# Optimization experiments

Measured on AMD Instinct MI355X. Metric: run time of the kernel, lower is better.

The kernel has to match this reference:

```python
import jax, jax.numpy as jnp
import numpy as np

V_PATCH_NUMS = (1, 2, 4, 6, 8, 10, 13, 16)
HW = 16
QUANT_RESI = 0.5
SHARE_K = 4
BETA = 1.0


def _pool_matrix(n_in, n_out):
    # adaptive average pooling as a [n_out, n_in] matrix (matches F.adaptive_avg_pool2d bins)
    P = np.zeros((n_out, n_in), np.float32)
    for i in range(n_out):
        s = (i * n_in) // n_out
        e = -((-(i + 1) * n_in) // n_out)  # ceil((i+1)*n_in/n_out)
        P[i, s:e] = 1.0 / (e - s)
    return jnp.asarray(P)


def _phi_index(si, SN):
    # PhiPartiallyShared.__getitem__(si/(SN-1)) with K=4 ticks
    K = SHARE_K
    ticks = np.linspace(1.0 / 3 / K, 1 - 1.0 / 3 / K, K) if K == 4 else np.linspace(1.0 / 2 / K, 1 - 1.0 / 2 / K, K)
    return int(np.argmin(np.abs(ticks - si / (SN - 1))))


def _phi(h, w, b):
    # Phi: h*(1-r) + conv3x3(h)*r, zero padding (nn.Conv2d default)
    y = jax.lax.conv_general_dilated(h, w, (1, 1), 'SAME',
                                     dimension_numbers=('NCHW', 'OIHW', 'NCHW'))
    y = y + b[None, :, None, None]
    return h * (1.0 - QUANT_RESI) + y * QUANT_RESI


def setup_inputs() -> dict:
    key = jax.random.key(0)
    k0, k1, k2 = jax.random.split(key, 3)
    B, C, V = 64, 32, 4096
    f = jax.random.normal(k0, (B, C, HW, HW), jnp.float32)
    embed = jax.random.normal(k1, (V, C), jnp.float32)  # EMAEmbedding.weight ~ randn
    phi_w = jax.random.normal(k2, (SHARE_K, C, C, 3, 3), jnp.float32) * (1.0 / np.sqrt(9.0 * C))
    phi_b = jnp.zeros((SHARE_K, C), jnp.float32)
    return {"f_BChw": f, "embed_weight": embed, "phi_w": phi_w, "phi_b": phi_b}


def reference(f_BChw, embed_weight, phi_w, phi_b):
    B, C, H, W = f_BChw.shape
    SN = len(V_PATCH_NUMS)
    f_ng = jax.lax.stop_gradient(f_BChw)
    f_hat = jnp.zeros_like(f_BChw)
    e_sq = jnp.sum(embed_weight * embed_weight, axis=1)  # [V]
    loss = jnp.float32(0.0)
    for si, pn in enumerate(V_PATCH_NUMS):
        rest = f_ng - jax.lax.stop_gradient(f_hat)  # residual to quantize (no grad through distance)
        if pn != H:
            P = _pool_matrix(H, pn)
            rest_d = jnp.einsum('oh,bchw,pw->bcop', P, rest, P)  # adaptive avg pool -> [B,C,pn,pn]
        else:
            rest_d = rest
        rest_NC = rest_d.transpose(0, 2, 3, 1).reshape(-1, C)  # [B*pn*pn, C]
        # squared euclidean cdist to codebook, argmin
        d = (jnp.sum(rest_NC * rest_NC, axis=1, keepdims=True)
             + e_sq[None, :]
             - 2.0 * (rest_NC @ embed_weight.T))  # [N, V]
        idx = jnp.argmin(d, axis=1)  # [B*pn*pn] int
        h = embed_weight[idx].reshape(B, pn, pn, C).transpose(0, 3, 1, 2)  # gather -> [B,C,pn,pn]
        if pn != H:
            h = jax.image.resize(h, (B, C, H, W), method='linear')  # bilinear, align_corners=False
        k = _phi_index(si, SN)
        h = _phi(h, phi_w[k], phi_b[k])
        f_hat = f_hat + h
        loss = loss + 0.25 * jnp.mean((jax.lax.stop_gradient(f_hat) - f_BChw) ** 2) \
                    + BETA * jnp.mean((f_hat - f_ng) ** 2)
    loss = loss / SN
    # straight-through estimator: grads flow to f_BChw as identity
    f_hat_st = jax.lax.stop_gradient(f_hat - f_BChw) + f_BChw
    return f_hat_st, loss
```

## Files before the change

kernel.cpp:

```cpp
#include <hip/hip_runtime.h>
#include <hip/hip_bf16.h>

#define BB 64
#define CC 32
#define HW2 256
#define VV 4096
#define NELEM (BB*CC*HW2)
#define PADW 18
#define PADA 324

#define OFF_F     0
#define OFF_FHAT  (OFF_F     + NELEM)
#define OFF_EMBT  (OFF_FHAT  + NELEM)
#define OFF_ESQ   (OFF_EMBT  + VV*CC)
#define OFF_PW    (OFF_ESQ   + VV)
#define OFF_PB    (OFF_PW    + 4*CC*CC*9)
#define OFF_REST  (OFF_PB    + 4*CC)
#define OFF_BESTA (OFF_REST  + 16384*CC)
#define OFF_BESTB (OFF_BESTA + 2*16384)
#define OFF_LOSS  (OFF_BESTB + 2*16384)
#define OFF_FLAG  (OFF_LOSS  + 1)
#define OFF_EMBR  (OFF_FLAG  + 1)
#define WS_NEED_EMBR ((OFF_EMBR + VV*CC) * 4)

__device__ __forceinline__ int embt_idx(int v, int c) {
    return (v >> 6) * 2048 + c * 64 + (v & 63);
}

__global__ void k_probe(const void* __restrict__ fin, int* __restrict__ flag) {
    __shared__ int cnt[256];
    int t = threadIdx.x;
    const __hip_bfloat16* p = (const __hip_bfloat16*)fin;
    int local = 0;
    for (int i = t; i < 8192; i += 256) {
        float v = __bfloat162float(p[i]);
        if (!(fabsf(v) < 1e3f)) local++;
    }
    cnt[t] = local;
    __syncthreads();
    for (int s = 128; s > 0; s >>= 1) {
        if (t < s) cnt[t] += cnt[t + s];
        __syncthreads();
    }
    if (t == 0) *flag = (cnt[0] >= 64) ? 1 : 0;
}

__global__ void k_prep(const void* __restrict__ fin,
                       const void* __restrict__ ein,
                       const void* __restrict__ win,
                       const void* __restrict__ bin_,
                       const int* __restrict__ flag,
                       float* __restrict__ f, float* __restrict__ fhat,
                       float* __restrict__ embT, float* __restrict__ pw,
                       float* __restrict__ pb, float* __restrict__ loss,
                       float* __restrict__ embR, int use_embR) {
    bool isf32 = (*flag != 0);
    int i = blockIdx.x * 256 + threadIdx.x;
    if (i < NELEM) {
        f[i] = isf32 ? ((const float*)fin)[i]
                     : __bfloat162float(((const __hip_bfloat16*)fin)[i]);
        fhat[i] = 0.f;
    }
    if (i < VV*CC) {
        float ev = isf32 ? ((const float*)ein)[i]
                         : __bfloat162float(((const __hip_bfloat16*)ein)[i]);
        int v = i >> 5, c = i & 31;
        embT[embt_idx(v, c)] = ev;
        if (use_embR) embR[i] = ev;
    }
    if (i < 4*CC*CC*9)
        pw[i] = isf32 ? ((const float*)win)[i]
                      : __bfloat162float(((const __hip_bfloat16*)win)[i]);
    if (i < 4*CC)
        pb[i] = isf32 ? ((const float*)bin_)[i]
                      : __bfloat162float(((const __hip_bfloat16*)bin_)[i]);
    if (i == 0) *loss = 0.f;
}

__global__ void k_esq(const float* __restrict__ embT, float* __restrict__ esq) {
    int v = blockIdx.x * 256 + threadIdx.x;
    if (v >= VV) return;
    const float* p = embT + (v >> 6) * 2048 + (v & 63);
    float s = 0.f;
    #pragma unroll
    for (int c = 0; c < CC; ++c) { float e = p[c * 64]; s = fmaf(e, e, s); }
    esq[v] = s;
}

__global__ void k_pool0(const float* __restrict__ f, const float* __restrict__ fhat,
                        float* __restrict__ rest, unsigned long long* __restrict__ best) {
    int n = threadIdx.x;
    int c = blockIdx.y;
    if (n >= BB) return;
    if (c == 0) best[n] = 0xFFFFFFFFFFFFFFFFull;
    const float* fb = f + (n * CC + c) * HW2;
    const float* hb = fhat + (n * CC + c) * HW2;
    float s = 0.f;
    for (int h = 0; h < 16; ++h)
        for (int w = 0; w < 16; ++w)
            s += fb[h * 16 + w] - hb[h * 16 + w];
    rest[n * CC + c] = s * (1.f / 256.f);
}

__global__ __launch_bounds__(256, 3)
void k_argmin_big(const float* __restrict__ rest, const float* __restrict__ embT,
                  const float* __restrict__ esq, unsigned long long* __restrict__ best,
                  int Ntot, int cpw) {
    __shared__ float xT[CC][132];
    __shared__ float eT[2 * CC * 64];
    __shared__ float xxs[2][128];
    int tid = threadIdx.x;
    int tx = tid & 15, ty = tid >> 4;
    int qblk = blockIdx.x * 128;
    int v0 = blockIdx.y * cpw;
    int t0 = v0 >> 6;

    {
        int q = tid >> 1, h = tid & 1;
        int qq = qblk + q; if (qq > Ntot - 1) qq = Ntot - 1;
        const float* xr = rest + qq * CC + h * 16;
        float part = 0.f;
        #pragma unroll
        for (int c = 0; c < 16; ++c) {
            float xv = xr[c];
            xT[h * 16 + c][q] = xv;
            part = fmaf(xv, xv, part);
        }
        xxs[h][q] = part;
    }
    __syncthreads();

    float xx[8];
    #pragma unroll
    for (int i = 0; i < 8; ++i) {
        int q = (i >> 2) * 64 + ty * 4 + (i & 3);
        xx[i] = xxs[0][q] + xxs[1][q];
    }

    float bd[8]; int bi[8];
    #pragma unroll
    for (int i = 0; i < 8; ++i) { bd[i] = 3.4e38f; bi[i] = v0; }

    int ntiles = cpw >> 7;
    for (int t = 0; t < ntiles; ++t) {
        int vbase = v0 + t * 128;
        const float* gt = embT + (size_t)(t0 + 2 * t) * 2048;
        float4 s0 = *(const float4*)(gt + tid * 4);
        float4 s1 = *(const float4*)(gt + 1024 + tid * 4);
        float4 s2 = *(const float4*)(gt + 2048 + tid * 4);
        float4 s3 = *(const float4*)(gt + 3072 + tid * 4);
        __syncthreads();
        *(float4*)(eT + tid * 4) = s0;
        *(float4*)(eT + 1024 + tid * 4) = s1;
        *(float4*)(eT + 2048 + tid * 4) = s2;
        *(float4*)(eT + 3072 + tid * 4) = s3;
        __syncthreads();

        float acc[8][8];
        #pragma unroll
        for (int i = 0; i < 8; ++i)
            #pragma unroll
            for (int j = 0; j < 8; ++j) acc[i][j] = 0.f;

        #pragma unroll 8
        for (int k = 0; k < CC; ++k) {
            float4 a0 = *(const float4*)&xT[k][ty * 4];
            float4 a1 = *(const float4*)&xT[k][64 + ty * 4];
            float4 b0 = *(const float4*)(eT + k * 64 + tx * 4);
            float4 b1 = *(const float4*)(eT + 2048 + k * 64 + tx * 4);
            float a[8] = {a0.x, a0.y, a0.z, a0.w, a1.x, a1.y, a1.z, a1.w};
            float b[8] = {b0.x, b0.y, b0.z, b0.w, b1.x, b1.y, b1.z, b1.w};
            #pragma unroll
            for (int i = 0; i < 8; ++i)
                #pragma unroll
                for (int j = 0; j < 8; ++j)
                    acc[i][j] = fmaf(a[i], b[j], acc[i][j]);
        }

        float4 e0 = *(const float4*)(esq + vbase + tx * 4);
        float4 e1 = *(const float4*)(esq + vbase + 64 + tx * 4);
        float es[8] = {e0.x, e0.y, e0.z, e0.w, e1.x, e1.y, e1.z, e1.w};
        #pragma unroll
        for (int i = 0; i < 8; ++i) {
            float base = xx[i];
            #pragma unroll
            for (int j = 0; j < 8; ++j) {
                float dist = fmaf(-2.f, acc[i][j], base + es[j]);
                int vidx = vbase + (j >> 2) * 64 + tx * 4 + (j & 3);
                if (dist < bd[i]) { bd[i] = dist; bi[i] = vidx; }
            }
        }
    }

    #pragma unroll
    for (int i = 0; i < 8; ++i) {
        unsigned u = __float_as_uint(bd[i]);
        unsigned long long mono = (u & 0x80000000u)
            ? (unsigned long long)(~u)
            : (unsigned long long)(u | 0x80000000u);
        unsigned long long pk = (mono << 32) | (unsigned long long)(unsigned)bi[i];
        #pragma unroll
        for (int m = 1; m <= 8; m <<= 1) {
            unsigned long long o = __shfl_xor(pk, m, 64);
            if (o < pk) pk = o;
        }
        int q = qblk + (i >> 2) * 64 + ty * 4 + (i & 3);
        if (tx == 0 && q < Ntot)
            atomicMin(best + q, pk);
    }
}

__global__ __launch_bounds__(256, 4)
void k_argmin_small(const float* __restrict__ rest, const float* __restrict__ embT,
                    const float* __restrict__ esq, unsigned long long* __restrict__ best,
                    int Ntot, int cpw) {
    int tid  = threadIdx.x;
    int w    = tid >> 6, lane = tid & 63;
    int q0   = blockIdx.x * 512 + w * 128 + lane;
    int q1   = q0 + 64;
    int v0   = blockIdx.y * cpw;

    bool act0 = (q0 < Ntot), act1 = (q1 < Ntot);
    if (!act0 && !act1) return;
    int qa = act0 ? q0 : (Ntot - 1);
    int qb = act1 ? q1 : (Ntot - 1);

    float a0v[32], a1v[32];
    {
        const float4* ra = (const float4*)(rest + qa * CC);
        const float4* rb = (const float4*)(rest + qb * CC);
        #pragma unroll
        for (int c4 = 0; c4 < 8; ++c4) {
            float4 va = ra[c4], vb4 = rb[c4];
            a0v[c4*4+0] = va.x;  a0v[c4*4+1] = va.y;
            a0v[c4*4+2] = va.z;  a0v[c4*4+3] = va.w;
            a1v[c4*4+0] = vb4.x; a1v[c4*4+1] = vb4.y;
            a1v[c4*4+2] = vb4.z; a1v[c4*4+3] = vb4.w;
        }
    }

    float p0a = 0.f, p1a = 0.f, p0b = 0.f, p1b = 0.f;
    #pragma unroll
    for (int c = 0; c < 16; ++c)  p0a = fmaf(a0v[c], a0v[c], p0a);
    #pragma unroll
    for (int c = 16; c < 32; ++c) p1a = fmaf(a0v[c], a0v[c], p1a);
    #pragma unroll
    for (int c = 0; c < 16; ++c)  p0b = fmaf(a1v[c], a1v[c], p0b);
    #pragma unroll
    for (int c = 16; c < 32; ++c) p1b = fmaf(a1v[c], a1v[c], p1b);
    float xx0 = p0a + p1a;
    float xx1 = p0b + p1b;

    float bd0 = 3.4e38f, bd1 = 3.4e38f;
    int   bi0 = v0,      bi1 = v0;

    int ntiles = cpw >> 3;
    for (int t = 0; t < ntiles; ++t) {
        int vb = v0 + t * 8;
        int boff = __builtin_amdgcn_readfirstlane((vb >> 6) * 2048 + (vb & 63));
        int eoff = __builtin_amdgcn_readfirstlane(vb);
        const float* bt = embT + boff;
        const float* ep = esq + eoff;

        float acc0[8], acc1[8];
        #pragma unroll
        for (int j = 0; j < 8; ++j) { acc0[j] = 0.f; acc1[j] = 0.f; }

        #pragma unroll
        for (int k = 0; k < CC; ++k) {
            float a0 = a0v[k], a1 = a1v[k];
            #pragma unroll
            for (int j = 0; j < 8; ++j) {
                float bv = bt[k * 64 + j];
                acc0[j] = fmaf(a0, bv, acc0[j]);
                acc1[j] = fmaf(a1, bv, acc1[j]);
            }
        }

        #pragma unroll
        for (int j = 0; j < 8; ++j) {
            float es = ep[j];
            float d0 = fmaf(-2.f, acc0[j], xx0 + es);
            if (d0 < bd0) { bd0 = d0; bi0 = vb + j; }
            float d1 = fmaf(-2.f, acc1[j], xx1 + es);
            if (d1 < bd1) { bd1 = d1; bi1 = vb + j; }
        }
    }

    unsigned u0 = __float_as_uint(bd0);
    unsigned long long mono0 = (u0 & 0x80000000u)
        ? (unsigned long long)(~u0)
        : (unsigned long long)(u0 | 0x80000000u);
    unsigned long long pk0 = (mono0 << 32) | (unsigned long long)(unsigned)bi0;
    unsigned u1 = __float_as_uint(bd1);
    unsigned long long mono1 = (u1 & 0x80000000u)
        ? (unsigned long long)(~u1)
        : (unsigned long long)(u1 | 0x80000000u);
    unsigned long long pk1 = (mono1 << 32) | (unsigned long long)(unsigned)bi1;

    if (act0) atomicMin(best + q0, pk0);
    if (act1) atomicMin(best + q1, pk1);
}

__global__ __launch_bounds__(256)
void k_fuse(const float* __restrict__ embT,
            const unsigned long long* __restrict__ best,
            const float* __restrict__ pw, const float* __restrict__ pb,
            const float* __restrict__ f, float* __restrict__ fhat,
            float* __restrict__ loss,
            float* __restrict__ rest,
            unsigned long long* __restrict__ best_next,
            const float* __restrict__ embR,
            int pn, int k, int pn_next) {
    __shared__ float h_pad[CC * PADA];
    __shared__ float extra[CC * 169];
    __shared__ float red[4];
    int b = blockIdx.x, co8 = blockIdx.y, t = threadIdx.x;
    int nn = pn * pn;
    int y = t >> 4, x = t & 15;

    for (int i = t; i < CC * 68; i += 256) {
        int c = i / 68, cell = i % 68;
        int yy, xx;
        if (cell < 18)      { yy = 0;  xx = cell; }
        else if (cell < 36) { yy = 17; xx = cell - 18; }
        else if (cell < 52) { yy = cell - 36 + 1; xx = 0; }
        else                { yy = cell - 52 + 1; xx = 17; }
        h_pad[c * PADA + yy * PADW + xx] = 0.f;
    }

    if (pn == 16) {
        int id = (int)(unsigned)(best[b * HW2 + t] & 0xFFFFFFFFull);
        int ctr = (y + 1) * PADW + (x + 1);
        if (embR) {
            const float4* er4 = (const float4*)(embR + id * CC);
            #pragma unroll
            for (int c4 = 0; c4 < 8; ++c4) {
                float4 v = er4[c4];
                h_pad[(c4*4+0) * PADA + ctr] = v.x;
                h_pad[(c4*4+1) * PADA + ctr] = v.y;
                h_pad[(c4*4+2) * PADA + ctr] = v.z;
                h_pad[(c4*4+3) * PADA + ctr] = v.w;
            }
        } else {
            const float* er = embT + (id >> 6) * 2048 + (id & 63);
            #pragma unroll
            for (int c = 0; c < CC; ++c)
                h_pad[c * PADA + ctr] = er[c * 64];
        }
    } else {
        float (*hs)[169] = (float(*)[169])extra;
        for (int cell = t; cell < nn; cell += 256) {
            int id = (int)(unsigned)(best[b * nn + cell] & 0xFFFFFFFFull);
            if (embR) {
                const float4* er4 = (const float4*)(embR + id * CC);
                #pragma unroll
                for (int c4 = 0; c4 < 8; ++c4) {
                    float4 v = er4[c4];
                    hs[c4*4+0][cell] = v.x;
                    hs[c4*4+1][cell] = v.y;
                    hs[c4*4+2][cell] = v.z;
                    hs[c4*4+3][cell] = v.w;
                }
            } else {
                const float* er = embT + (id >> 6) * 2048 + (id & 63);
                #pragma unroll
                for (int c = 0; c < CC; ++c) hs[c][cell] = er[c * 64];
            }
        }
        __syncthreads();
        float scale = (float)pn / 16.f;
        float sy = (y + 0.5f) * scale - 0.5f;
        sy = fminf(fmaxf(sy, 0.f), (float)(pn - 1));
        int y0 = (int)sy; int y1 = min(y0 + 1, pn - 1); float wy = sy - (float)y0;
        float sx = (x + 0.5f) * scale - 0.5f;
        sx = fminf(fmaxf(sx, 0.f), (float)(pn - 1));
        int x0 = (int)sx; int x1 = min(x0 + 1, pn - 1); float wx = sx - (float)x0;
        float wy0 = 1.f - wy, wx0 = 1.f - wx;
        int ctr = (y + 1) * PADW + (x + 1);
        #pragma unroll
        for (int c = 0; c < CC; ++c) {
            float v00 = hs[c][y0 * pn + x0], v01 = hs[c][y0 * pn + x1];
            float v10 = hs[c][y1 * pn + x0], v11 = hs[c][y1 * pn + x1];
            float a0 = wy0 * v00 + wy * v10;
            float a1 = wy0 * v01 + wy * v11;
            h_pad[c * PADA + ctr] = wx0 * a0 + wx * a1;
        }
    }
    __syncthreads();

    int wv  = t >> 6, lane = t & 63;
    int cg  = wv & 1;
    int pg  = (wv >> 1) * 64 + lane;
    int cy  = pg >> 3, cx0 = (pg & 7) * 2;
    int cob = co8 * 4 + cg * 2;
    int wuni = __builtin_amdgcn_readfirstlane(k * CC + cob);
    const float* wpk = pw + wuni * (CC * 9);

    float acc00 = 0.f, acc01 = 0.f, acc10 = 0.f, acc11 = 0.f;
    const float* hb0 = h_pad + cy * PADW + cx0;
    #pragma unroll
    for (int ci_ = 0; ci_ < CC; ++ci_) {
        float win[3][4];
        #pragma unroll
        for (int dy = 0; dy < 3; ++dy) {
            float2 r0 = *(const float2*)(hb0 + ci_ * PADA + dy * PADW);
            float2 r1 = *(const float2*)(hb0 + ci_ * PADA + dy * PADW + 2);
            win[dy][0] = r0.x; win[dy][1] = r0.y;
            win[dy][2] = r1.x; win[dy][3] = r1.y;
        }
        const float* w0 = wpk + ci_ * 9;
        const float* w1 = wpk + CC * 9 + ci_ * 9;
        #pragma unroll
        for (int q = 0; q < 9; ++q) {
            int dy = q / 3, dx = q % 3;
            float wv0 = w0[q], wv1 = w1[q];
            acc00 = fmaf(win[dy][dx],     wv0, acc00);
            acc01 = fmaf(win[dy][dx],     wv1, acc01);
            acc10 = fmaf(win[dy][dx + 1], wv0, acc10);
            acc11 = fmaf(win[dy][dx + 1], wv1, acc11);
        }
    }

    float* diff = extra;
    float lsum = 0.f;
    {
        int ctrc = (cy + 1) * PADW + (cx0 + 1);
        #pragma unroll
        for (int oo = 0; oo < 2; ++oo) {
            int co = cob + oo;
            float bias = pb[k * CC + co];
            float a0 = oo ? acc01 : acc00;
            float a1 = oo ? acc11 : acc10;
            int pos = (b * CC + co) * HW2 + cy * 16 + cx0;
            float2 fh2 = *(float2*)(fhat + pos);
            float2 f2  = *(const float2*)(f + pos);
            float hv0 = h_pad[co * PADA + ctrc];
            float hv1 = h_pad[co * PADA + ctrc + 1];
            float out0 = hv0 * 0.5f + (a0 + bias) * 0.5f;
            float out1 = hv1 * 0.5f + (a1 + bias) * 0.5f;
            fh2.x += out0; fh2.y += out1;
            *(float2*)(fhat + pos) = fh2;
            float dd0 = f2.x - fh2.x;
            float dd1 = f2.y - fh2.y;
            int dbase = (cg * 2 + oo) * HW2 + cy * 16 + cx0;
            diff[dbase]     = dd0;
            diff[dbase + 1] = dd1;
            lsum = fmaf(dd0, dd0, lsum);
            lsum = fmaf(dd1, dd1, lsum);
        }
    }
    #pragma unroll
    for (int off = 32; off > 0; off >>= 1) lsum += __shfl_down(lsum, off, 64);
    if ((t & 63) == 0) red[t >> 6] = lsum;
    __syncthreads();
    if (t == 0)
        atomicAdd(loss, red[0] + red[1] + red[2] + red[3]);

    if (pn_next > 0) {
        int nn2 = pn_next * pn_next;
        for (int q = t; q < nn2 * 4; q += 256) {
            int cell = q % nn2, o = q / nn2;
            int i = cell / pn_next, j = cell % pn_next;
            int s0 = (i * 16) / pn_next, e0 = ((i + 1) * 16 + pn_next - 1) / pn_next;
            int s1 = (j * 16) / pn_next, e1 = ((j + 1) * 16 + pn_next - 1) / pn_next;
            float inv = 1.f / (float)((e0 - s0) * (e1 - s1));
            float s = 0.f;
            for (int h = s0; h < e0; ++h)
                for (int w = s1; w < e1; ++w)
                    s += diff[o * HW2 + h * 16 + w];
            rest[(b * nn2 + cell) * CC + co8 * 4 + o] = s * inv;
        }
        if (co8 == 0)
            for (int q = t; q < nn2; q += 256)
                best_next[b * nn2 + q] = 0xFFFFFFFFFFFFFFFFull;
    }
}

__global__ void k_out(const float* __restrict__ fhat, const float* __restrict__ loss,
                      const int* __restrict__ flag, void* __restrict__ out) {
    bool isf32 = (*flag != 0);
    int i = blockIdx.x * 256 + threadIdx.x;
    if (i > NELEM) return;
    float v;
    if (i < NELEM) v = fhat[i];
    else           v = (*loss) * (1.25f / (float)NELEM / 8.f);
    if (isf32) ((float*)out)[i] = v;
    else       ((__hip_bfloat16*)out)[i] = __float2bfloat16(v);
}

extern "C" void kernel_launch(void* const* d_in, const int* in_sizes, int n_in,
                              void* d_out, int out_size, void* d_ws, size_t ws_size,
                              hipStream_t stream) {
    const void* fin  = d_in[0];
    const void* ein  = d_in[1];
    const void* win  = d_in[2];
    const void* bin_ = d_in[3];
    float* ws = (float*)d_ws;
    float* f    = ws + OFF_F;
    float* fhat = ws + OFF_FHAT;
    float* embT = ws + OFF_EMBT;
    float* esq  = ws + OFF_ESQ;
    float* pw   = ws + OFF_PW;
    float* pb   = ws + OFF_PB;
    float* rest = ws + OFF_REST;
    unsigned long long* bestA = (unsigned long long*)(ws + OFF_BESTA);
    unsigned long long* bestB = (unsigned long long*)(ws + OFF_BESTB);
    float* loss = ws + OFF_LOSS;
    int*   flag = (int*)(ws + OFF_FLAG);
    int use_embR = (ws_size >= (size_t)WS_NEED_EMBR) ? 1 : 0;
    float* embR = use_embR ? (ws + OFF_EMBR) : nullptr;

    static const int PN[8] = {1, 2, 4, 6, 8, 10, 13, 16};
    static const int KK[8] = {0, 0, 1, 1, 2, 2, 3, 3};
    static const int SPs[4] = {512, 512, 512, 256};
    static const int SPb[4] = {16, 16, 8, 8};

    k_probe<<<1, 256, 0, stream>>>(fin, flag);
    k_prep<<<(NELEM + 255) / 256, 256, 0, stream>>>(fin, ein, win, bin_, flag,
                                                    f, fhat, embT, pw, pb, loss,
                                                    embR, use_embR);
    k_esq<<<(VV + 255) / 256, 256, 0, stream>>>(embT, esq);
    k_pool0<<<dim3(1, CC), 256, 0, stream>>>(f, fhat, rest, bestA);

    for (int si = 0; si < 8; ++si) {
        int pn = PN[si];
        int Ntot = BB * pn * pn;
        unsigned long long* bcur = (si & 1) ? bestB : bestA;
        unsigned long long* bnxt = (si & 1) ? bestA : bestB;
        int pn_next = (si < 7) ? PN[si + 1] : 0;
        if (si < 4) {
            int Sp = SPs[si];
            int cpw = VV / Sp;
            int gx = (Ntot + 511) / 512;
            k_argmin_small<<<dim3(gx, Sp), 256, 0, stream>>>(rest, embT, esq, bcur,
                                                             Ntot, cpw);
        } else {
            int Sp = SPb[si - 4];
            int cpw = VV / Sp;
            int gx = (Ntot + 127) / 128;
            k_argmin_big<<<dim3(gx, Sp), 256, 0, stream>>>(rest, embT, esq, bcur,
                                                           Ntot, cpw);
        }
        k_fuse<<<dim3(BB, 8), 256, 0, stream>>>(embT, bcur, pw, pb, f, fhat, loss,
                                                rest, bnxt, embR, pn, KK[si], pn_next);
    }
    k_out<<<(NELEM + 1 + 255) / 256, 256, 0, stream>>>(fhat, loss, flag, d_out);
}
```

Before: 449.3 us.

## Merge per-scale kernel sequence into one persistent cooperative kernel with grid syncs

Replaces the eighteen or so separate launches (esq, pool0, per-scale argmin and fuse, output) with a single cooperative persistent kernel. Blocks loop over virtual block indices and use grid-wide syncs between stages, removing launch gaps and per-launch overhead. If the cooperative launch fails, the code falls back to the original multi-kernel path. In exchange, grid size is capped by occupancy (at most 512 blocks, launch bounds of 2 per CU) and shared memory is sized for the largest stage, which could lower parallelism in the argmin stages relative to the original large grids.

```diff
diff --git a/kernel.cpp b/kernel.cpp
--- a/kernel.cpp
+++ b/kernel.cpp
@@ -1,5 +1,8 @@
 #include <hip/hip_runtime.h>
 #include <hip/hip_bf16.h>
+#include <hip/hip_cooperative_groups.h>
+
+namespace cg = cooperative_groups;
 
 #define BB 64
 #define CC 32
@@ -22,6 +25,9 @@
 #define OFF_FLAG  (OFF_LOSS  + 1)
 #define OFF_EMBR  (OFF_FLAG  + 1)
 #define WS_NEED_EMBR ((OFF_EMBR + VV*CC) * 4)
+
+#define ARG_SMEM  (CC*132 + 2*CC*64 + 256)
+#define FUSE_SMEM (CC*PADA + CC*169 + 8)
 
 __device__ __forceinline__ int embt_idx(int v, int c) {
     return (v >> 6) * 2048 + c * 64 + (v & 63);
@@ -77,20 +83,25 @@
     if (i == 0) *loss = 0.f;
 }
 
-__global__ void k_esq(const float* __restrict__ embT, float* __restrict__ esq) {
-    int v = blockIdx.x * 256 + threadIdx.x;
-    if (v >= VV) return;
-    const float* p = embT + (v >> 6) * 2048 + (v & 63);
-    float s = 0.f;
-    #pragma unroll
-    for (int c = 0; c < CC; ++c) { float e = p[c * 64]; s = fmaf(e, e, s); }
-    esq[v] = s;
-}
-
-__global__ void k_pool0(const float* __restrict__ f, const float* __restrict__ fhat,
-                        float* __restrict__ rest, unsigned long long* __restrict__ best) {
+
+__device__ __forceinline__ void dev_esq(const float* __restrict__ embT,
+                                        float* __restrict__ esq,
+                                        int g0, int gs) {
+    for (int v = g0; v < VV; v += gs) {
+        const float* p = embT + (v >> 6) * 2048 + (v & 63);
+        float s = 0.f;
+        #pragma unroll
+        for (int c = 0; c < CC; ++c) { float e = p[c * 64]; s = fmaf(e, e, s); }
+        esq[v] = s;
+    }
+}
+
+__device__ __forceinline__ void dev_pool0(const float* __restrict__ f,
+                                          const float* __restrict__ fhat,
+                                          float* __restrict__ rest,
+                                          unsigned long long* __restrict__ best,
+                                          int c) {
     int n = threadIdx.x;
-    int c = blockIdx.y;
     if (n >= BB) return;
     if (c == 0) best[n] = 0xFFFFFFFFFFFFFFFFull;
     const float* fb = f + (n * CC + c) * HW2;
@@ -102,18 +113,21 @@
     rest[n * CC + c] = s * (1.f / 256.f);
 }
 
-__global__ __launch_bounds__(256, 3)
-void k_argmin_big(const float* __restrict__ rest, const float* __restrict__ embT,
-                  const float* __restrict__ esq, unsigned long long* __restrict__ best,
-                  int Ntot, int cpw) {
-    __shared__ float xT[CC][132];
-    __shared__ float eT[2 * CC * 64];
-    __shared__ float xxs[2][128];
+__device__ __forceinline__ void dev_argmin_big(
+        int bx, int by,
+        const float* __restrict__ rest, const float* __restrict__ embT,
+        const float* __restrict__ esq, unsigned long long* __restrict__ best,
+        int Ntot, int cpw, float* __restrict__ smem) {
+    float (*xT)[132] = (float(*)[132])smem;
+    float* eT  = smem + CC * 132;
+    float* xxs = smem + CC * 132 + 2 * CC * 64;
     int tid = threadIdx.x;
     int tx = tid & 15, ty = tid >> 4;
-    int qblk = blockIdx.x * 128;
-    int v0 = blockIdx.y * cpw;
+    int qblk = bx * 128;
+    int v0 = by * cpw;
     int t0 = v0 >> 6;
+
+    __syncthreads();
 
     {
         int q = tid >> 1, h = tid & 1;
@@ -126,7 +140,7 @@
             xT[h * 16 + c][q] = xv;
             part = fmaf(xv, xv, part);
         }
-        xxs[h][q] = part;
+        xxs[h * 128 + q] = part;
     }
     __syncthreads();
 
@@ -134,7 +148,7 @@
     #pragma unroll
     for (int i = 0; i < 8; ++i) {
         int q = (i >> 2) * 64 + ty * 4 + (i & 3);
-        xx[i] = xxs[0][q] + xxs[1][q];
+        xx[i] = xxs[q] + xxs[128 + q];
     }
 
     float bd[8]; int bi[8];
@@ -210,15 +224,16 @@
     }
 }
 
-__global__ __launch_bounds__(256, 4)
-void k_argmin_small(const float* __restrict__ rest, const float* __restrict__ embT,
-                    const float* __restrict__ esq, unsigned long long* __restrict__ best,
-                    int Ntot, int cpw) {
+__device__ __forceinline__ void dev_argmin_small(
+        int bx, int by,
+        const float* __restrict__ rest, const float* __restrict__ embT,
+        const float* __restrict__ esq, unsigned long long* __restrict__ best,
+        int Ntot, int cpw) {
     int tid  = threadIdx.x;
     int w    = tid >> 6, lane = tid & 63;
-    int q0   = blockIdx.x * 512 + w * 128 + lane;
+    int q0   = bx * 512 + w * 128 + lane;
     int q1   = q0 + 64;
-    int v0   = blockIdx.y * cpw;
+    int v0   = by * cpw;
 
     bool act0 = (q0 < Ntot), act1 = (q1 < Ntot);
     if (!act0 && !act1) return;
@@ -302,22 +317,24 @@
     if (act1) atomicMin(best + q1, pk1);
 }
 
-__global__ __launch_bounds__(256)
-void k_fuse(const float* __restrict__ embT,
-            const unsigned long long* __restrict__ best,
-            const float* __restrict__ pw, const float* __restrict__ pb,
-            const float* __restrict__ f, float* __restrict__ fhat,
-            float* __restrict__ loss,
-            float* __restrict__ rest,
-            unsigned long long* __restrict__ best_next,
-            const float* __restrict__ embR,
-            int pn, int k, int pn_next) {
-    __shared__ float h_pad[CC * PADA];
-    __shared__ float extra[CC * 169];
-    __shared__ float red[4];
-    int b = blockIdx.x, co8 = blockIdx.y, t = threadIdx.x;
+__device__ __forceinline__ void dev_fuse(
+        int b, int co8,
+        const float* __restrict__ embT,
+        const unsigned long long* __restrict__ best,
+        const float* __restrict__ pw, const float* __restrict__ pb,
+        const float* __restrict__ f, float* __restrict__ fhat,
+        float* __restrict__ loss, float* __restrict__ rest,
+        unsigned long long* __restrict__ best_next,
+        const float* __restrict__ embR,
+        int pn, int k, int pn_next, float* __restrict__ smem) {
+    float* h_pad = smem;
+    float* extra = smem + CC * PADA;
+    float* red   = smem + CC * PADA + CC * 169;
+    int t = threadIdx.x;
     int nn = pn * pn;
     int y = t >> 4, x = t & 15;
+
+    __syncthreads();
 
     for (int i = t; i < CC * 68; i += 256) {
         int c = i / 68, cell = i % 68;
@@ -390,10 +407,10 @@
     __syncthreads();
 
     int wv  = t >> 6, lane = t & 63;
-    int cg  = wv & 1;
+    int cg_ = wv & 1;
     int pg  = (wv >> 1) * 64 + lane;
     int cy  = pg >> 3, cx0 = (pg & 7) * 2;
-    int cob = co8 * 4 + cg * 2;
+    int cob = co8 * 4 + cg_ * 2;
     int wuni = __builtin_amdgcn_readfirstlane(k * CC + cob);
     const float* wpk = pw + wuni * (CC * 9);
 
@@ -443,7 +460,7 @@
             *(float2*)(fhat + pos) = fh2;
             float dd0 = f2.x - fh2.x;
             float dd1 = f2.y - fh2.y;
-            int dbase = (cg * 2 + oo) * HW2 + cy * 16 + cx0;
+            int dbase = (cg_ * 2 + oo) * HW2 + cy * 16 + cx0;
             diff[dbase]     = dd0;
             diff[dbase + 1] = dd1;
             lsum = fmaf(dd0, dd0, lsum);
@@ -477,16 +494,116 @@
     }
 }
 
+__device__ __forceinline__ void dev_out(const float* __restrict__ fhat,
+                                        const float* __restrict__ loss,
+                                        const int* __restrict__ flag,
+                                        void* __restrict__ out,
+                                        int g0, int gs) {
+    bool isf32 = (*flag != 0);
+    for (int i = g0; i <= NELEM; i += gs) {
+        float v;
+        if (i < NELEM) v = fhat[i];
+        else           v = (*loss) * (1.25f / (float)NELEM / 8.f);
+        if (isf32) ((float*)out)[i] = v;
+        else       ((__hip_bfloat16*)out)[i] = __float2bfloat16(v);
+    }
+}
+
+__global__ __launch_bounds__(256, 2)
+void k_coop(const float* __restrict__ f, float* __restrict__ fhat,
+            const float* __restrict__ embT, float* __restrict__ esq,
+            const float* __restrict__ pw, const float* __restrict__ pb,
+            float* __restrict__ rest,
+            unsigned long long* __restrict__ bestA,
+            unsigned long long* __restrict__ bestB,
+            float* __restrict__ loss, const int* __restrict__ flag,
+            const float* __restrict__ embR, void* __restrict__ out) {
+    cg::grid_group grid = cg::this_grid();
+    __shared__ float smem[FUSE_SMEM];
+    int bid = blockIdx.x, G = gridDim.x, tid = threadIdx.x;
+
+    const int PN[8]  = {1, 2, 4, 6, 8, 10, 13, 16};
+    const int KK[8]  = {0, 0, 1, 1, 2, 2, 3, 3};
+    const int SPs[4] = {512, 512, 512, 256};
+    const int SPb[4] = {16, 16, 8, 8};
+
+    dev_esq(embT, esq, bid * 256 + tid, G * 256);
+    for (int c = bid; c < CC; c += G)
+        dev_pool0(f, fhat, rest, bestA, c);
+    __threadfence(); grid.sync(); __threadfence();
+
+    for (int si = 0; si < 8; ++si) {
+        int pn = PN[si];
+        int Ntot = BB * pn * pn;
+        unsigned long long* bcur = (si & 1) ? bestB : bestA;
+        unsigned long long* bnxt = (si & 1) ? bestA : bestB;
+        int pn_next = (si < 7) ? PN[si + 1] : 0;
+
+        if (si < 4) {
+            int Sp = SPs[si], cpw = VV / Sp;
+            int gx = (Ntot + 511) / 512, NV = gx * Sp;
+            for (int vb = bid; vb < NV; vb += G)
+                dev_argmin_small(vb % gx, vb / gx, rest, embT, esq, bcur,
+                                 Ntot, cpw);
+        } else {
+            int Sp = SPb[si - 4], cpw = VV / Sp;
+            int gx = (Ntot + 127) / 128, NV = gx * Sp;
+            for (int vb = bid; vb < NV; vb += G)
+                dev_argmin_big(vb % gx, vb / gx, rest, embT, esq, bcur,
+                               Ntot, cpw, smem);
+        }
+        __threadfence(); grid.sync(); __threadfence();
+
+        for (int vb = bid; vb < BB * 8; vb += G)
+            dev_fuse(vb >> 3, vb & 7, embT, bcur, pw, pb, f, fhat, loss,
+                     rest, bnxt, embR, pn, KK[si], pn_next, smem);
+        __threadfence(); grid.sync(); __threadfence();
+    }
+
+    dev_out(fhat, loss, flag, out, bid * 256 + tid, G * 256);
+}
+
+__global__ void k_esq(const float* __restrict__ embT, float* __restrict__ esq) {
+    dev_esq(embT, esq, blockIdx.x * 256 + threadIdx.x, gridDim.x * 256);
+}
+
+__global__ void k_pool0(const float* __restrict__ f, const float* __restrict__ fhat,
+                        float* __restrict__ rest, unsigned long long* __restrict__ best) {
+    dev_pool0(f, fhat, rest, best, blockIdx.y);
+}
+
+__global__ __launch_bounds__(256, 3)
+void k_argmin_big(const float* __restrict__ rest, const float* __restrict__ embT,
+                  const float* __restrict__ esq, unsigned long long* __restrict__ best,
+                  int Ntot, int cpw) {
+    __shared__ float smem[ARG_SMEM];
+    dev_argmin_big(blockIdx.x, blockIdx.y, rest, embT, esq, best, Ntot, cpw, smem);
+}
+
+__global__ __launch_bounds__(256, 4)
+void k_argmin_small(const float* __restrict__ rest, const float* __restrict__ embT,
+                    const float* __restrict__ esq, unsigned long long* __restrict__ best,
+                    int Ntot, int cpw) {
+    dev_argmin_small(blockIdx.x, blockIdx.y, rest, embT, esq, best, Ntot, cpw);
+}
+
+__global__ __launch_bounds__(256)
+void k_fuse(const float* __restrict__ embT,
+            const unsigned long long* __restrict__ best,
+            const float* __restrict__ pw, const float* __restrict__ pb,
+            const float* __restrict__ f, float* __restrict__ fhat,
+            float* __restrict__ loss, float* __restrict__ rest,
+            unsigned long long* __restrict__ best_next,
+            const float* __restrict__ embR,
+            int pn, int k, int pn_next) {
+    __shared__ float smem[FUSE_SMEM];
+    dev_fuse(blockIdx.x, blockIdx.y, embT, best, pw, pb, f, fhat, loss,
+             rest, best_next, embR, pn, k, pn_next, smem);
+}
+
 __global__ void k_out(const float* __restrict__ fhat, const float* __restrict__ loss,
                       const int* __restrict__ flag, void* __restrict__ out) {
-    bool isf32 = (*flag != 0);
-    int i = blockIdx.x * 256 + threadIdx.x;
-    if (i > NELEM) return;
-    float v;
-    if (i < NELEM) v = fhat[i];
-    else           v = (*loss) * (1.25f / (float)NELEM / 8.f);
-    if (isf32) ((float*)out)[i] = v;
-    else       ((__hip_bfloat16*)out)[i] = __float2bfloat16(v);
+    dev_out(fhat, loss, flag, out, blockIdx.x * 256 + threadIdx.x, gridDim.x * 256);
 }
 
 extern "C" void kernel_launch(void* const* d_in, const int* in_sizes, int n_in,
@@ -511,39 +628,65 @@
     int use_embR = (ws_size >= (size_t)WS_NEED_EMBR) ? 1 : 0;
     float* embR = use_embR ? (ws + OFF_EMBR) : nullptr;
 
-    static const int PN[8] = {1, 2, 4, 6, 8, 10, 13, 16};
-    static const int KK[8] = {0, 0, 1, 1, 2, 2, 3, 3};
-    static const int SPs[4] = {512, 512, 512, 256};
-    static const int SPb[4] = {16, 16, 8, 8};
-
     k_probe<<<1, 256, 0, stream>>>(fin, flag);
     k_prep<<<(NELEM + 255) / 256, 256, 0, stream>>>(fin, ein, win, bin_, flag,
                                                     f, fhat, embT, pw, pb, loss,
                                                     embR, use_embR);
-    k_esq<<<(VV + 255) / 256, 256, 0, stream>>>(embT, esq);
-    k_pool0<<<dim3(1, CC), 256, 0, stream>>>(f, fhat, rest, bestA);
-
-    for (int si = 0; si < 8; ++si) {
-        int pn = PN[si];
-        int Ntot = BB * pn * pn;
-        unsigned long long* bcur = (si & 1) ? bestB : bestA;
-        unsigned long long* bnxt = (si & 1) ? bestA : bestB;
-        int pn_next = (si < 7) ? PN[si + 1] : 0;
-        if (si < 4) {
-            int Sp = SPs[si];
-            int cpw = VV / Sp;
-            int gx = (Ntot + 511) / 512;
-            k_argmin_small<<<dim3(gx, Sp), 256, 0, stream>>>(rest, embT, esq, bcur,
-                                                             Ntot, cpw);
-        } else {
-            int Sp = SPb[si - 4];
-            int cpw = VV / Sp;
-            int gx = (Ntot + 127) / 128;
-            k_argmin_big<<<dim3(gx, Sp), 256, 0, stream>>>(rest, embT, esq, bcur,
-                                                           Ntot, cpw);
-        }
-        k_fuse<<<dim3(BB, 8), 256, 0, stream>>>(embT, bcur, pw, pb, f, fhat, loss,
-                                                rest, bnxt, embR, pn, KK[si], pn_next);
-    }
-    k_out<<<(NELEM + 1 + 255) / 256, 256, 0, stream>>>(fhat, loss, flag, d_out);
-}
+
+    static int gmax = -1;
+    if (gmax < 0) {
+        int bpc = 0;
+        if (hipOccupancyMaxActiveBlocksPerMultiprocessor(
+                &bpc, reinterpret_cast<const void*>(k_coop), 256, 0) != hipSuccess
+            || bpc < 1)
+            bpc = 1;
+        int ncu = 256;
+        hipDeviceProp_t prop;
+        if (hipGetDeviceProperties(&prop, 0) == hipSuccess &&
+            prop.multiProcessorCount > 0)
+            ncu = prop.multiProcessorCount;
+        long long g = (long long)bpc * ncu;
+        if (g > 512) g = 512;
+        if (g < 64)  g = 64;
+        gmax = (int)g;
+    }
+
+    void* args[] = { &f, &fhat, &embT, &esq, &pw, &pb, &rest,
+                     &bestA, &bestB, &loss, &flag, &embR, &d_out };
+    hipError_t cerr = hipLaunchCooperativeKernel(
+        reinterpret_cast<void*>(k_coop), dim3(gmax), dim3(256), args, 0, stream);
+
+    if (cerr != hipSuccess) {
+        static const int PN[8] = {1, 2, 4, 6, 8, 10, 13, 16};
+        static const int KK[8] = {0, 0, 1, 1, 2, 2, 3, 3};
+        static const int SPs[4] = {512, 512, 512, 256};
+        static const int SPb[4] = {16, 16, 8, 8};
+
+        k_esq<<<(VV + 255) / 256, 256, 0, stream>>>(embT, esq);
+        k_pool0<<<dim3(1, CC), 256, 0, stream>>>(f, fhat, rest, bestA);
+        for (int si = 0; si < 8; ++si) {
+            int pn = PN[si];
+            int Ntot = BB * pn * pn;
+            unsigned long long* bcur = (si & 1) ? bestB : bestA;
+            unsigned long long* bnxt = (si & 1) ? bestA : bestB;
+            int pn_next = (si < 7) ? PN[si + 1] : 0;
+            if (si < 4) {
+                int Sp = SPs[si];
+                int cpw = VV / Sp;
+                int gx = (Ntot + 511) / 512;
+                k_argmin_small<<<dim3(gx, Sp), 256, 0, stream>>>(rest, embT, esq,
+                                                                 bcur, Ntot, cpw);
+            } else {
+                int Sp = SPb[si - 4];
+                int cpw = VV / Sp;
+                int gx = (Ntot + 127) / 128;
+                k_argmin_big<<<dim3(gx, Sp), 256, 0, stream>>>(rest, embT, esq,
+                                                               bcur, Ntot, cpw);
+            }
+            k_fuse<<<dim3(BB, 8), 256, 0, stream>>>(embT, bcur, pw, pb, f, fhat,
+                                                    loss, rest, bnxt, embR,
+                                                    pn, KK[si], pn_next);
+        }
+        k_out<<<(NELEM + 1 + 255) / 256, 256, 0, stream>>>(fhat, loss, flag, d_out);
+    }
+}
```

After: 1.629 ms. 3.62x slower.
